# Kernel optimization log

Hardware: AMD Instinct MI355X
Metric: run time of the kernel (lower is better)

The kernel has to match this reference:

```python
import jax, jax.numpy as jnp
import numpy as np

N = 2048; E = 32768; E2 = 65536; B = 8; P = 20; M = B * P * P * P
NR = 16; SH = 9; FEAT = NR * SH; RE = 64; RH = 128; MC = 32; MH = 16; MODES = 10; CUT = 5.0


def _sh(u):
    # real spherical harmonics l=0,1,2, e3nn 'integral' normalization, on unit vectors u[...,3]
    x, y, z = u[..., 0], u[..., 1], u[..., 2]
    c0 = 0.28209479177387814  # 1/(2 sqrt(pi))
    c1 = 0.4886025119029199   # sqrt(3/(4 pi))
    l0 = jnp.full(x.shape, c0, dtype=u.dtype)
    return jnp.stack([
        l0,
        c1 * y, c1 * z, c1 * x,
        1.0925484305920792 * x * y,
        1.0925484305920792 * y * z,
        0.31539156525252005 * (3.0 * z * z - 1.0),
        1.0925484305920792 * x * z,
        0.5462742152960396 * (x * x - y * y),
    ], axis=-1)


def _gauss(r):
    # soft_one_hot_linspace(basis='gaussian', cutoff=False) * sqrt(RE)
    vals = jnp.linspace(0.0, CUT, RE)
    step = vals[1] - vals[0]
    d = (r[:, None] - vals) / step
    return jnp.exp(-d * d) / 1.12 * np.sqrt(RE)


def _norm_act(x):
    # NormActivation over irreps 16x0e + 16x1 + 16x2 (layout [16 | 16*3 | 16*5])
    s = x[:, :NR]
    v = x[:, NR:NR * 4].reshape(-1, NR, 3)
    t = x[:, NR * 4:].reshape(-1, NR, 5)
    s = s * jax.nn.sigmoid(jnp.abs(s))
    v = v * jax.nn.sigmoid(jnp.linalg.norm(v, axis=-1))[..., None]
    t = t * jax.nn.sigmoid(jnp.linalg.norm(t, axis=-1))[..., None]
    return jnp.concatenate([s, v.reshape(-1, NR * 3), t.reshape(-1, NR * 5)], axis=-1)


def _rmlp(e, m1, m2, m3):
    h = jax.nn.silu(e @ m1)
    h = jax.nn.silu(h @ m2)
    return h @ m3


def _gcn(src, dst, x, sh, emb_e, W, m1, m2, m3, n_dst, Wsc=None):
    # fully-connected tensor-product message passing: gather -> outer(feat, sh) -> GEMM
    # -> radial gate -> scatter-sum; optional self-connection
    xs = x[src]                                                    # [E, Cin]
    msg = (xs[:, :, None] * sh[:, None, :]).reshape(xs.shape[0], -1) @ W
    msg = msg * _rmlp(emb_e, m1, m2, m3)
    out = jax.ops.segment_sum(msg, dst, num_segments=n_dst)
    return out if Wsc is None else out + x @ Wsc


def _spec(x, wr, wi):
    # FNO-style 3D spectral conv on [B,P,P,P,C], low MODES kept in 4 corner blocks
    Px = x.shape[1]
    xf = jnp.fft.rfftn(x, axes=(1, 2, 3))
    w = wr + 1j * wi                                              # [4,C,C,m,m,m]
    m = MODES
    of = jnp.zeros(xf.shape, dtype=xf.dtype)
    corners = [(slice(0, m), slice(0, m)), (slice(-m, None), slice(0, m)),
               (slice(0, m), slice(-m, None)), (slice(-m, None), slice(-m, None))]
    for k, (s1, s2) in enumerate(corners):
        blk = jnp.einsum('bxyzi,ioxyz->bxyzo', xf[:, s1, s2, :m, :], w[k])
        of = of.at[:, s1, s2, :m, :].set(blk)
    return jnp.fft.irfftn(of, s=(Px, Px, Px), axes=(1, 2, 3))


def _forward(pos, cell, emb, g0_W, g0_Wsc, g0_m1, g0_m2, g0_m3,
             g12_W, g12_Wsc, g12_m1, g12_m2, g12_m3,
             a2m_W, a2m_m1, a2m_m2, a2m_m3,
             m2a_W, m2a_m1, m2a_m2, m2a_m3,
             fc0_W, fc0_b, sw_r, sw_i, pw, ff1, ff2, fc1, fc2,
             atomic_numbers, batch, edge_src, edge_dst, atom_src, mesh_dst):
    # atom-atom spherical GCN stack
    ev = pos[edge_src] - pos[edge_dst]
    el = jnp.linalg.norm(ev, axis=-1) + 1e-8
    sh_e = _sh(ev / el[:, None])
    emb_e = _gauss(el)
    x = emb[atomic_numbers]                                        # [N, NR]
    x = _gcn(edge_src, edge_dst, x, sh_e, emb_e, g0_W, g0_m1, g0_m2, g0_m3, N, g0_Wsc)
    for i in range(2):
        x = _norm_act(x)
        x = _gcn(edge_src, edge_dst, x, sh_e, emb_e, g12_W[i], g12_m1[i], g12_m2[i], g12_m3[i], N, g12_Wsc[i])
    # particle mesh positions per cell
    fr = jnp.arange(P) / P
    fg = jnp.stack(jnp.meshgrid(fr, fr, fr, indexing='ij'), axis=-1)   # [P,P,P,3]
    meshpos = jnp.einsum('xyzk,bkl->bxyzl', fg, cell).reshape(-1, 3)   # [M,3]
    # atom -> mesh conv
    ev2 = meshpos[mesh_dst] - pos[atom_src]
    el2 = jnp.linalg.norm(ev2, axis=-1) + 1e-8
    sh2 = _sh(ev2 / el2[:, None])
    emb2 = _gauss(el2)
    mf = _gcn(atom_src, mesh_dst, x, sh2, emb2, a2m_W, a2m_m1, a2m_m2, a2m_m3, M)   # [M, MC]
    mf = mf * jax.nn.sigmoid(jnp.abs(mf))                          # NormActivation on 0e
    mf = mf.reshape(B, P, P, P, MC)
    # PME / FNO mesh conv
    grid = jnp.broadcast_to(fg, (B, P, P, P, 3))
    h = jnp.concatenate([mf, grid], axis=-1) @ fc0_W + fc0_b       # lift to width MH
    for l in range(3):
        h = jax.nn.gelu(_spec(h, sw_r[l], sw_i[l]) + h @ pw[l])
        h = h + jax.nn.gelu(h @ ff1[l]) @ ff2[l]                   # using_ff branch
    h = jax.nn.gelu(h @ fc1) @ fc2                                 # [B,P,P,P,MH]
    mf2 = h.reshape(-1, MH)
    # mesh -> atom conv, per-atom energy, readout
    af = _gcn(mesh_dst, atom_src, mf2, sh2, emb2, m2a_W, m2a_m1, m2a_m2, m2a_m3, N)  # [N,1]
    return jax.ops.segment_sum(af, batch, num_segments=B)          # [B,1]


def setup_inputs():
    key = jax.random.key(0)
    ks = jax.random.split(key, 40)
    r = lambda i, shape, scale: jax.random.normal(ks[i], shape, dtype=jnp.float32) * scale
    inp = {}
    inp['pos'] = jax.random.uniform(ks[0], (N, 3), dtype=jnp.float32) * 10.0
    inp['cell'] = jnp.eye(3, dtype=jnp.float32)[None] * 10.0 + r(1, (B, 3, 3), 0.05)
    inp['atomic_numbers'] = jax.random.randint(ks[2], (N,), 1, 100)
    inp['batch'] = jnp.sort(jax.random.randint(ks[3], (N,), 0, B))
    inp['edge_src'] = jax.random.randint(ks[4], (E,), 0, N)
    inp['edge_dst'] = jax.random.randint(ks[5], (E,), 0, N)
    inp['atom_src'] = jax.random.randint(ks[6], (E2,), 0, N)
    inp['mesh_dst'] = jax.random.randint(ks[7], (E2,), 0, M)
    inp['emb'] = r(8, (100, NR), 1.0)
    inp['g0_W'] = r(9, (NR * SH, FEAT), (NR * SH) ** -0.5)
    inp['g0_Wsc'] = r(10, (NR, FEAT), NR ** -0.5)
    inp['g0_m1'] = r(11, (RE, RH), RE ** -0.5)
    inp['g0_m2'] = r(12, (RH, RH), RH ** -0.5)
    inp['g0_m3'] = r(13, (RH, FEAT), RH ** -0.5)
    inp['g12_W'] = r(14, (2, FEAT * SH, FEAT), (FEAT * SH) ** -0.5)
    inp['g12_Wsc'] = r(15, (2, FEAT, FEAT), FEAT ** -0.5)
    inp['g12_m1'] = r(16, (2, RE, RH), RE ** -0.5)
    inp['g12_m2'] = r(17, (2, RH, RH), RH ** -0.5)
    inp['g12_m3'] = r(18, (2, RH, FEAT), RH ** -0.5)
    inp['a2m_W'] = r(19, (FEAT * SH, MC), (FEAT * SH) ** -0.5)
    inp['a2m_m1'] = r(20, (RE, RH), RE ** -0.5)
    inp['a2m_m2'] = r(21, (RH, RH), RH ** -0.5)
    inp['a2m_m3'] = r(22, (RH, MC), RH ** -0.5)
    inp['m2a_W'] = r(23, (MH * SH, 1), (MH * SH) ** -0.5)
    inp['m2a_m1'] = r(24, (RE, RH), RE ** -0.5)
    inp['m2a_m2'] = r(25, (RH, RH), RH ** -0.5)
    inp['m2a_m3'] = r(26, (RH, 1), RH ** -0.5)
    inp['fc0_W'] = r(27, (MC + 3, MH), (MC + 3) ** -0.5)
    inp['fc0_b'] = jnp.zeros((MH,), dtype=jnp.float32)
    inp['sw_r'] = r(28, (3, 4, MH, MH, MODES, MODES, MODES), 1.0 / MH)
    inp['sw_i'] = r(29, (3, 4, MH, MH, MODES, MODES, MODES), 1.0 / MH)
    inp['pw'] = r(30, (3, MH, MH), MH ** -0.5)
    inp['ff1'] = r(31, (3, MH, 4 * MH), MH ** -0.5)
    inp['ff2'] = r(32, (3, 4 * MH, MH), (4 * MH) ** -0.5)
    inp['fc1'] = r(33, (MH, 128), MH ** -0.5)
    inp['fc2'] = r(34, (128, MH), 128 ** -0.5)
    return inp


def reference(pos, cell, emb, g0_W, g0_Wsc, g0_m1, g0_m2, g0_m3, g12_W, g12_Wsc, g12_m1, g12_m2, g12_m3, a2m_W, a2m_m1, a2m_m2, a2m_m3, m2a_W, m2a_m1, m2a_m2, m2a_m3, fc0_W, fc0_b, sw_r, sw_i, pw, ff1, ff2, fc1, fc2, atomic_numbers, batch, edge_src, edge_dst, atom_src, mesh_dst):
    return _forward(pos, cell, emb, g0_W, g0_Wsc, g0_m1, g0_m2, g0_m3, g12_W, g12_Wsc, g12_m1, g12_m2, g12_m3, a2m_W, a2m_m1, a2m_m2, a2m_m3, m2a_W, m2a_m1, m2a_m2, m2a_m3, fc0_W, fc0_b, sw_r, sw_i, pw, ff1, ff2, fc1, fc2, atomic_numbers, batch, edge_src, edge_dst, atom_src, mesh_dst)
```

## Files before the change

### kernel.cpp

```cpp
#include <hip/hip_runtime.h>
#include <math.h>

#define DEVI __device__ __forceinline__

namespace {

constexpr int N_  = 2048;
constexpr int E_  = 32768;
constexpr int E2_ = 65536;
constexpr int M_  = 64000;
constexpr int NT_ = 2048;
constexpr float TMAX_ = 5.5f;
constexpr float TH_ = TMAX_ / NT_;

DEVI float sigm(float x)  { return 1.0f/(1.0f+expf(-x)); }
DEVI float geluf(float x) {
  float t = tanhf(0.7978845608028654f*(x + 0.044715f*x*x*x));
  return 0.5f*x*(1.0f+t);
}

__global__ void zero_k(float* __restrict__ p, int n){
  int i = blockIdx.x*256 + threadIdx.x;
  if (i < n) p[i] = 0.0f;
}

__global__ void meshpos_k(const float* __restrict__ cell, float* __restrict__ mp){
  int m = blockIdx.x*256 + threadIdx.x;
  if (m >= M_) return;
  int b = m/8000, r = m%8000;
  float fx = (float)(r/400)    * 0.05f;
  float fy = (float)((r/20)%20)* 0.05f;
  float fz = (float)(r%20)     * 0.05f;
  const float* c = cell + b*9;
  mp[(size_t)m*3+0] = fx*c[0] + fy*c[3] + fz*c[6];
  mp[(size_t)m*3+1] = fx*c[1] + fy*c[4] + fz*c[7];
  mp[(size_t)m*3+2] = fx*c[2] + fy*c[5] + fz*c[8];
}

__global__ void edge_geom2_k(const float* __restrict__ Ppos, const int* __restrict__ pi,
                             const float* __restrict__ Qpos, const int* __restrict__ qi,
                             float* __restrict__ sh, float* __restrict__ el_out, int nE){
  int e = blockIdx.x*256 + threadIdx.x;
  if (e >= nE) return;
  int a = pi[e], b = qi[e];
  float ex = Ppos[(size_t)a*3+0] - Qpos[(size_t)b*3+0];
  float ey = Ppos[(size_t)a*3+1] - Qpos[(size_t)b*3+1];
  float ez = Ppos[(size_t)a*3+2] - Qpos[(size_t)b*3+2];
  float el = sqrtf(ex*ex+ey*ey+ez*ez) + 1e-8f;
  el_out[e] = el;
  float x = ex/el, y = ey/el, z = ez/el;
  float* s = sh + (size_t)e*9;
  s[0] = 0.28209479177387814f;
  s[1] = 0.4886025119029199f*y;
  s[2] = 0.4886025119029199f*z;
  s[3] = 0.4886025119029199f*x;
  s[4] = 1.0925484305920792f*x*y;
  s[5] = 1.0925484305920792f*y*z;
  s[6] = 0.31539156525252005f*(3.0f*z*z-1.0f);
  s[7] = 1.0925484305920792f*x*z;
  s[8] = 0.5462742152960396f*(x*x-y*y);
}

__global__ void gather_emb_k(const float* __restrict__ emb, const int* __restrict__ an,
                             float* __restrict__ x16){
  int idx = blockIdx.x*256 + threadIdx.x;
  if (idx >= N_*16) return;
  int n = idx >> 4, f = idx & 15;
  x16[idx] = emb[(size_t)an[n]*16 + f];
}

__global__ void es_k(float* __restrict__ Es){
  int idx = blockIdx.x*256 + threadIdx.x;
  if (idx >= NT_*64) return;
  int r = idx >> 6, k = idx & 63;
  const float step = 5.0f/63.0f;
  float d = (r*TH_ - k*step)/step;
  Es[idx] = expf(-d*d)*(8.0f/1.12f);
}

DEVI float lerp_tab(const float* __restrict__ T, float el, int O, int o){
  float u = el * (1.0f/TH_);
  u = fminf(u, (float)(NT_-1));
  int i = (int)u; if (i > NT_-2) i = NT_-2;
  float f = u - (float)i;
  float t0 = T[(size_t)i*O + o];
  float t1 = T[(size_t)(i+1)*O + o];
  return t0 + f*(t1 - t0);
}

struct BG {
  const float* A[5]; const float* B[5]; float* C[5];
  int K; int Nc[5];
};
template<int ACT>
__global__ __launch_bounds__(256) void bgemm_k(BG args){
  int chain = blockIdx.z;
  const float* A = args.A[chain];
  const float* Bm = args.B[chain];
  float* C = args.C[chain];
  int K = args.K, Nc = args.Nc[chain];
  int row0 = blockIdx.y*64, col0 = blockIdx.x*64;
  if (col0 >= Nc) return;
  __shared__ float As[16][72];
  __shared__ float Bs[16][72];
  int tid = threadIdx.x;
  int tx = tid & 15, ty = tid >> 4;
  float acc[4][4] = {};
  for (int k0 = 0; k0 < K; k0 += 16) {
    { int kk = tid & 15; int mloc = tid >> 4;
      int gk = k0 + kk;
      #pragma unroll
      for (int p = 0; p < 4; ++p) {
        int m = mloc + p*16; int gm = row0 + m;
        As[kk][m] = A[(size_t)gm*K + gk];
      } }
    { int nn = tid & 63; int kl = tid >> 6;
      #pragma unroll
      for (int p = 0; p < 4; ++p) {
        int kk = kl + p*4; int gk = k0 + kk; int gn = col0 + nn;
        Bs[kk][nn] = (gn < Nc) ? Bm[(size_t)gk*Nc + gn] : 0.0f;
      } }
    __syncthreads();
    #pragma unroll
    for (int kk = 0; kk < 16; ++kk) {
      float4 a4 = *(const float4*)&As[kk][ty*4];
      float4 b4 = *(const float4*)&Bs[kk][tx*4];
      float a[4] = {a4.x,a4.y,a4.z,a4.w};
      float b[4] = {b4.x,b4.y,b4.z,b4.w};
      #pragma unroll
      for (int i=0;i<4;++i)
        #pragma unroll
        for (int j=0;j<4;++j) acc[i][j] += a[i]*b[j];
    }
    __syncthreads();
  }
  for (int i=0;i<4;++i) {
    int gm = row0 + ty*4+i;
    for (int j=0;j<4;++j) {
      int gn = col0 + tx*4+j; if (gn >= Nc) continue;
      float v = acc[i][j];
      if (ACT==1) v = v*sigm(v);
      C[(size_t)gm*Nc + gn] = v;
    }
  }
}

__global__ __launch_bounds__(256) void gemm128_k(const float* __restrict__ A, const float* __restrict__ B,
                        float* __restrict__ C, int Mr, int K, int Nc){
  __shared__ float As[16][72];
  __shared__ float Bs[16][136];
  int tid = threadIdx.x;
  int row0 = blockIdx.y*64, col0 = blockIdx.x*128;
  int tx = tid & 15, ty = tid >> 4;
  float acc[4][8] = {};
  for (int k0 = 0; k0 < K; k0 += 16) {
    {
      int kk = tid & 15, mloc = tid >> 4;
      int gk = k0 + kk;
      #pragma unroll
      for (int p = 0; p < 4; ++p) {
        int m = mloc + p*16; int gm = row0 + m;
        As[kk][m] = (gm < Mr) ? A[(size_t)gm*K + gk] : 0.0f;
      }
    }
    {
      int nn4 = tid & 31, kk = tid >> 5;
      #pragma unroll
      for (int p = 0; p < 2; ++p) {
        int kkk = kk + p*8;
        int gk = k0 + kkk;
        int gn = col0 + nn4*4;
        float4 v = make_float4(0.f,0.f,0.f,0.f);
        if (gn + 3 < Nc) {
          v = *(const float4*)(B + (size_t)gk*Nc + gn);
        } else if (gn < Nc) {
          float t0 = B[(size_t)gk*Nc + gn];
          float t1 = (gn+1<Nc)? B[(size_t)gk*Nc + gn+1] : 0.f;
          float t2 = (gn+2<Nc)? B[(size_t)gk*Nc + gn+2] : 0.f;
          v = make_float4(t0,t1,t2,0.f);
        }
        *(float4*)&Bs[kkk][nn4*4] = v;
      }
    }
    __syncthreads();
    #pragma unroll
    for (int kk = 0; kk < 16; ++kk) {
      float4 a4 = *(const float4*)&As[kk][ty*4];
      float4 b0 = *(const float4*)&Bs[kk][tx*8];
      float4 b1 = *(const float4*)&Bs[kk][tx*8+4];
      float av[4] = {a4.x,a4.y,a4.z,a4.w};
      float bv[8] = {b0.x,b0.y,b0.z,b0.w,b1.x,b1.y,b1.z,b1.w};
      #pragma unroll
      for (int i=0;i<4;++i)
        #pragma unroll
        for (int j=0;j<8;++j) acc[i][j] += av[i]*bv[j];
    }
    __syncthreads();
  }
  for (int i=0;i<4;++i){
    int gm = row0 + ty*4 + i; if (gm >= Mr) continue;
    for (int j=0;j<8;++j){
      int gn = col0 + tx*8 + j; if (gn >= Nc) continue;
      C[(size_t)gm*Nc + gn] = acc[i][j];
    }
  }
}

template<int O>
__global__ void wreshape_k(const float* __restrict__ W, float* __restrict__ Wt, int F){
  int idx = blockIdx.x*256 + threadIdx.x;
  int total = F*9*O;
  if (idx >= total) return;
  int o = idx % O; int s = (idx / O) % 9; int f = idx / (9*O);
  Wt[idx] = W[(size_t)(f*9+s)*O + o];
}

template<int O>
__global__ void econtract_k(const float* __restrict__ Y, const int* __restrict__ src,
                            const int* __restrict__ dst, const float* __restrict__ SH,
                            const float* __restrict__ EL, const float* __restrict__ T,
                            float* __restrict__ out, int nE){
  int idx = blockIdx.x*256 + threadIdx.x;
  if (idx >= nE*O) return;
  int e = idx / O, o = idx - e*O;
  const float* sr = SH + (size_t)e*9;
  const float* yr = Y + (size_t)src[e]*(9*O) + o;
  float acc = 0.0f;
  #pragma unroll
  for (int s = 0; s < 9; ++s) acc += sr[s] * yr[s*O];
  float rv = lerp_tab(T, EL[e], O, o);
  atomicAdd(&out[(size_t)dst[e]*O + o], acc * rv);
}

__global__ void normact_k(const float* __restrict__ x, float* __restrict__ y){
  int idx = blockIdx.x*256 + threadIdx.x;
  if (idx >= N_*16) return;
  int n = idx >> 4, r = idx & 15;
  const float* xr = x + (size_t)n*144;
  float* yr = y + (size_t)n*144;
  float s = xr[r];
  yr[r] = s * sigm(fabsf(s));
  float v0 = xr[16+r*3], v1 = xr[16+r*3+1], v2 = xr[16+r*3+2];
  float gv = sigm(sqrtf(v0*v0+v1*v1+v2*v2));
  yr[16+r*3]=v0*gv; yr[16+r*3+1]=v1*gv; yr[16+r*3+2]=v2*gv;
  float t0=xr[64+r*5],t1=xr[64+r*5+1],t2=xr[64+r*5+2],t3=xr[64+r*5+3],t4=xr[64+r*5+4];
  float gt = sigm(sqrtf(t0*t0+t1*t1+t2*t2+t3*t3+t4*t4));
  yr[64+r*5]=t0*gt; yr[64+r*5+1]=t1*gt; yr[64+r*5+2]=t2*gt; yr[64+r*5+3]=t3*gt; yr[64+r*5+4]=t4*gt;
}

__global__ void fc0_k(const float* __restrict__ mf, const float* __restrict__ Wt,
                      const float* __restrict__ bb, float* __restrict__ h){
  int idx = blockIdx.x*256 + threadIdx.x;
  if (idx >= M_*16) return;
  int m = idx >> 4, o = idx & 15;
  int r = m % 8000;
  float fx = (float)(r/400)*0.05f, fy = (float)((r/20)%20)*0.05f, fz = (float)(r%20)*0.05f;
  const float* mfr = mf + (size_t)m*32;
  float acc = bb[o];
  #pragma unroll
  for (int j=0;j<32;++j){
    float v = mfr[j];
    v = v * sigm(fabsf(v));
    acc += v*Wt[j*16+o];
  }
  acc += fx*Wt[32*16+o] + fy*Wt[33*16+o] + fz*Wt[34*16+o];
  h[idx] = acc;
}

__global__ __launch_bounds__(256) void wreorder2_k(const float* __restrict__ wr, const float* __restrict__ wi,
                          float2* __restrict__ W2){
  __shared__ float2 tile[2560];
  int l = blockIdx.y;
  const float* wrl = wr + (size_t)l*1024000;
  const float* wil = wi + (size_t)l*1024000;
  int p = blockIdx.x;
  int ky = p/20, kx = p%20;
  int corner = ((kx>=10)?1:0) + ((ky>=10)?2:0);
  int base2 = corner*256;
  int soff = (kx%10)*100 + (ky%10)*10;
  for (int t = threadIdx.x; t < 2560; t += 256){
    int chunk = t/10, kz = t - chunk*10;
    size_t src = (size_t)(base2 + chunk)*1000 + soff + kz;
    tile[kz*256 + chunk] = make_float2(wrl[src], wil[src]);
  }
  __syncthreads();
  float2* dst = W2 + (size_t)l*1024000 + (size_t)p*2560;
  for (int t = threadIdx.x; t < 2560; t += 256) dst[t] = tile[t];
}

__global__ __launch_bounds__(256) void zyfwd_k(const float* __restrict__ h, float2* __restrict__ cA){
  __shared__ float  pl[20][20][4];
  __shared__ float2 tz[20][10][4];
  __shared__ float2 tw[20];
  int tid = threadIdx.x;
  if (tid < 20){ float a = -6.283185307179586f*tid/20.0f; tw[tid] = make_float2(cosf(a), sinf(a)); }
  int bid = blockIdx.x;
  int b = bid / 80, rem = bid % 80;
  int X = rem >> 2, cg = rem & 3;
  const float* hp = h + (size_t)(b*20+X)*400*16 + cg*4;
  for (int t = tid; t < 400; t += 256) {
    int y = t/20, z = t%20;
    const float4 v = *(const float4*)(hp + (size_t)t*16);
    pl[y][z][0]=v.x; pl[y][z][1]=v.y; pl[y][z][2]=v.z; pl[y][z][3]=v.w;
  }
  __syncthreads();
  for (int t = tid; t < 800; t += 256) {
    int c = t & 3, kz = (t>>2)%10, y = t/40;
    float sr=0.0f, si=0.0f; int j=0;
    for (int z=0; z<20; ++z){
      float v = pl[y][z][c];
      float2 w = tw[j];
      sr += v*w.x; si += v*w.y;
      j += kz; if (j>=20) j-=20;
    }
    tz[y][kz][c] = make_float2(sr,si);
  }
  __syncthreads();
  for (int t = tid; t < 800; t += 256) {
    int c = t & 3, kz = (t>>2)%10, ky = t/40;
    float sr=0.0f, si=0.0f; int j=0;
    for (int y=0; y<20; ++y){
      float2 v = tz[y][kz][c];
      float2 w = tw[j];
      sr += v.x*w.x - v.y*w.y;
      si += v.x*w.y + v.y*w.x;
      j += ky; if (j>=20) j-=20;
    }
    cA[((size_t)((b*20+ky)*10+kz)*20 + X)*16 + cg*4+c] = make_float2(sr,si);
  }
}

__global__ __launch_bounds__(256) void xmix_k(const float2* __restrict__ cA, float2* __restrict__ cB,
                    const float2* __restrict__ W2){
  __shared__ float2 xin[16][20];
  __shared__ float2 Xf[20][16];
  __shared__ float2 Mx[20][16];
  __shared__ float2 twf[20], twi[20];
  int tid = threadIdx.x;
  if (tid < 20){
    float a = -6.283185307179586f*tid/20.0f;
    twf[tid] = make_float2(cosf(a), sinf(a));
    twi[tid] = make_float2(cosf(a), -sinf(a));
  }
  int bid = blockIdx.x;
  int b = bid/200, rem = bid%200;
  int ky = rem/10, kz = rem%10;
  const float2* src = cA + (size_t)((b*20+ky)*10+kz)*320;
  for (int t = tid; t < 320; t += 256){
    int x = t/16, i = t%16;
    xin[i][x] = src[t];
  }
  __syncthreads();
  for (int t = tid; t < 320; t += 256){
    int kx = t/16, i = t%16;
    float sr=0.0f, si=0.0f; int j=0;
    for (int x=0;x<20;++x){
      float2 v = xin[i][x]; float2 w = twf[j];
      sr += v.x*w.x - v.y*w.y; si += v.x*w.y + v.y*w.x;
      j += kx; if (j>=20) j-=20;
    }
    Xf[kx][i] = make_float2(sr,si);
  }
  __syncthreads();
  for (int t = tid; t < 320; t += 256){
    int kx = t/16, o = t%16;
    const float2* wp = W2 + ((size_t)(ky*20+kx)*10 + kz)*256 + o;
    float sr=0.0f, si=0.0f;
    #pragma unroll
    for (int i=0;i<16;++i){
      float2 a = Xf[kx][i];
      float2 w = wp[i*16];
      sr += a.x*w.x - a.y*w.y;
      si += a.x*w.y + a.y*w.x;
    }
    Mx[kx][o] = make_float2(sr,si);
  }
  __syncthreads();
  for (int t = tid; t < 320; t += 256){
    int x = t/16, o = t%16;
    float sr=0.0f, si=0.0f; int j=0;
    for (int kx=0;kx<20;++kx){
      float2 v = Mx[kx][o]; float2 w = twi[j];
      sr += v.x*w.x - v.y*w.y; si += v.x*w.y + v.y*w.x;
      j += x; if (j>=20) j-=20;
    }
    cB[((size_t)((b*20+x)*20+ky)*10+kz)*16 + o] = make_float2(sr,si);
  }
}

__global__ __launch_bounds__(256) void yzinv_k(const float2* __restrict__ cB, float* __restrict__ spec){
  __shared__ float2 ci[20][10][4];
  __shared__ float2 ty[20][10][4];
  __shared__ float2 twi[20];
  int tid = threadIdx.x;
  if (tid < 20){ float a = 6.283185307179586f*tid/20.0f; twi[tid] = make_float2(cosf(a), sinf(a)); }
  int bid = blockIdx.x;
  int b = bid/80, rem = bid%80;
  int X = rem>>2, cg = rem&3;
  const float2* src = cB + (size_t)(b*20+X)*200*16;
  for (int t = tid; t < 800; t += 256){
    int c = t&3, kz = (t>>2)%10, ky = t/40;
    ci[ky][kz][c] = src[(size_t)(ky*10+kz)*16 + cg*4+c];
  }
  __syncthreads();
  for (int t = tid; t < 800; t += 256){
    int c = t&3, kz = (t>>2)%10, y = t/40;
    float sr=0.0f, si=0.0f; int j=0;
    for (int ky=0;ky<20;++ky){
      float2 v = ci[ky][kz][c]; float2 w = twi[j];
      sr += v.x*w.x - v.y*w.y; si += v.x*w.y + v.y*w.x;
      j += y; if (j>=20) j-=20;
    }
    ty[y][kz][c] = make_float2(sr,si);
  }
  __syncthreads();
  float* dst = spec + (size_t)(b*20+X)*400*16 + cg*4;
  for (int t = tid; t < 1600; t += 256){
    int c = t&3, z = (t>>2)%20, y = t/80;
    float acc = ty[y][0][c].x;
    float a2 = 0.0f; int jj = 0;
    for (int kz=1; kz<10; ++kz){
      jj += z; if (jj>=20) jj-=20;
      float2 v = ty[y][kz][c]; float2 w = twi[jj];
      a2 += v.x*w.x - v.y*w.y;
    }
    acc += 2.0f*a2;
    dst[(size_t)(y*20+z)*16 + c] = acc * (1.0f/8000.0f);
  }
}

__global__ __launch_bounds__(256) void ffn3_k(const float* __restrict__ spec, const float* __restrict__ h,
                     const float* __restrict__ pw, const float* __restrict__ ff1,
                     const float* __restrict__ ff2, float* __restrict__ hout){
  __shared__ float spw[256];
  __shared__ float sf1[1024];
  __shared__ float sf2[1024];
  __shared__ float h2s[128][17];
  __shared__ float red[2][128][17];
  int tid = threadIdx.x;
  spw[tid] = pw[tid];
  for (int t = tid; t < 1024; t += 256){ sf1[t]=ff1[t]; sf2[t]=ff2[t]; }
  int rl = tid >> 1, q = tid & 1;
  int m = blockIdx.x*128 + rl;
  const float* hr = h + (size_t)m*16;
  float hl[16];
  #pragma unroll
  for (int i=0;i<16;++i) hl[i] = hr[i];
  __syncthreads();
  const float* sp = spec + (size_t)m*16;
  #pragma unroll
  for (int c=0;c<8;++c){
    int o = q*8+c;
    float acc = sp[o];
    #pragma unroll
    for (int i=0;i<16;++i) acc += hl[i]*spw[i*16+o];
    h2s[rl][o] = geluf(acc);
  }
  __syncthreads();
  float h2l[16];
  #pragma unroll
  for (int i=0;i<16;++i) h2l[i] = h2s[rl][i];
  float part[16] = {};
  for (int kk=0;kk<32;++kk){
    int k = q*32+kk;
    float a0=0.0f, a1=0.0f;
    #pragma unroll
    for (int i=0;i<8;++i){ a0 += h2l[i]*sf1[i*64+k]; a1 += h2l[8+i]*sf1[(8+i)*64+k]; }
    float tk = geluf(a0+a1);
    #pragma unroll
    for (int o=0;o<16;++o) part[o] += tk*sf2[k*16+o];
  }
  #pragma unroll
  for (int o=0;o<16;++o) red[q][rl][o] = part[o];
  __syncthreads();
  #pragma unroll
  for (int c=0;c<8;++c){
    int o = q*8+c;
    hout[(size_t)m*16+o] = h2s[rl][o] + red[0][rl][o] + red[1][rl][o];
  }
}

__global__ __launch_bounds__(256) void fctail3_k(const float* __restrict__ h, const float* __restrict__ fc1,
                        const float* __restrict__ fc2, float* __restrict__ outm){
  __shared__ float s1[2048];
  __shared__ float s2[2048];
  __shared__ float red[2][128][17];
  int tid = threadIdx.x;
  for (int t = tid; t < 2048; t += 256){ s1[t]=fc1[t]; s2[t]=fc2[t]; }
  int rl = tid >> 1, q = tid & 1;
  int m = blockIdx.x*128 + rl;
  const float* hr = h + (size_t)m*16;
  float hl[16];
  #pragma unroll
  for (int i=0;i<16;++i) hl[i] = hr[i];
  __syncthreads();
  float part[16] = {};
  for (int kk=0;kk<64;++kk){
    int k = q*64+kk;
    float a0=0.0f, a1=0.0f;
    #pragma unroll
    for (int i=0;i<8;++i){ a0 += hl[i]*s1[i*128+k]; a1 += hl[8+i]*s1[(8+i)*128+k]; }
    float tk = geluf(a0+a1);
    #pragma unroll
    for (int o=0;o<16;++o) part[o] += tk*s2[k*16+o];
  }
  #pragma unroll
  for (int o=0;o<16;++o) red[q][rl][o] = part[o];
  __syncthreads();
  #pragma unroll
  for (int c=0;c<8;++c){
    int o = q*8+c;
    outm[(size_t)m*16+o] = red[0][rl][o] + red[1][rl][o];
  }
}

__global__ void m2a_k(const float* __restrict__ mf2, const int* __restrict__ mdst,
                      const int* __restrict__ asrc, const float* __restrict__ sh2,
                      const float* __restrict__ Wt, const float* __restrict__ EL,
                      const float* __restrict__ T, float* __restrict__ af){
  int e = blockIdx.x*256 + threadIdx.x;
  if (e >= E2_) return;
  const float* xr = mf2 + (size_t)mdst[e]*16;
  const float* sr = sh2 + (size_t)e*9;
  float sh[9];
  #pragma unroll
  for (int s=0;s<9;++s) sh[s] = sr[s];
  float acc = 0.0f;
  #pragma unroll
  for (int f=0;f<16;++f) {
    float xv = xr[f];
    float dot = 0.0f;
    #pragma unroll
    for (int s=0;s<9;++s) dot += sh[s]*Wt[f*9+s];
    acc += xv*dot;
  }
  float rv = lerp_tab(T, EL[e], 1, 0);
  atomicAdd(&af[asrc[e]], acc*rv);
}

__global__ void bsum_k(const float* __restrict__ af, const int* __restrict__ batch,
                       float* __restrict__ out){
  int n = blockIdx.x*256 + threadIdx.x;
  if (n >= N_) return;
  atomicAdd(&out[batch[n]], af[n]);
}

}

extern "C" void kernel_launch(void* const* d_in, const int* in_sizes, int n_in,
                              void* d_out, int out_size, void* d_ws, size_t ws_size,
                              hipStream_t stream) {
  (void)in_sizes; (void)n_in; (void)out_size; (void)ws_size;
  const float* pos   = (const float*)d_in[0];
  const float* cell  = (const float*)d_in[1];
  const int*   an    = (const int*)d_in[2];
  const int*   batch = (const int*)d_in[3];
  const int*   esrc  = (const int*)d_in[4];
  const int*   edst  = (const int*)d_in[5];
  const int*   asrc  = (const int*)d_in[6];
  const int*   mdst  = (const int*)d_in[7];
  const float* emb   = (const float*)d_in[8];
  const float* g0_W  = (const float*)d_in[9];
  const float* g0_Wsc= (const float*)d_in[10];
  const float* g0_m1 = (const float*)d_in[11];
  const float* g0_m2 = (const float*)d_in[12];
  const float* g0_m3 = (const float*)d_in[13];
  const float* g12_W = (const float*)d_in[14];
  const float* g12_Wsc=(const float*)d_in[15];
  const float* g12_m1= (const float*)d_in[16];
  const float* g12_m2= (const float*)d_in[17];
  const float* g12_m3= (const float*)d_in[18];
  const float* a2m_W = (const float*)d_in[19];
  const float* a2m_m1= (const float*)d_in[20];
  const float* a2m_m2= (const float*)d_in[21];
  const float* a2m_m3= (const float*)d_in[22];
  const float* m2a_W = (const float*)d_in[23];
  const float* m2a_m1= (const float*)d_in[24];
  const float* m2a_m2= (const float*)d_in[25];
  const float* m2a_m3= (const float*)d_in[26];
  const float* fc0_W = (const float*)d_in[27];
  const float* fc0_b = (const float*)d_in[28];
  const float* sw_r  = (const float*)d_in[29];
  const float* sw_i  = (const float*)d_in[30];
  const float* pw    = (const float*)d_in[31];
  const float* ff1   = (const float*)d_in[32];
  const float* ff2   = (const float*)d_in[33];
  const float* fc1   = (const float*)d_in[34];
  const float* fc2   = (const float*)d_in[35];
  float* out = (float*)d_out;

  float* Wp = (float*)d_ws;
  size_t off = 0;
  auto alloc = [&](size_t n){ float* p = Wp + off; off += n; return p; };
  float* meshpos = alloc((size_t)M_*3);
  float* she   = alloc((size_t)E_*9);
  float* ELe   = alloc((size_t)E_);
  float* sh2   = alloc((size_t)E2_*9);
  float* EL2   = alloc((size_t)E2_);
  float* x16   = alloc((size_t)N_*16);
  float* xatom = alloc((size_t)N_*144);
  float* xact  = alloc((size_t)N_*144);
  float* Wt    = alloc((size_t)144*1296);
  float* Yg    = alloc((size_t)N_*1296);
  float* mf    = alloc((size_t)M_*32);
  float* hbuf  = alloc((size_t)M_*16);
  float* htmp  = alloc((size_t)M_*16);
  float2* cA   = (float2*)alloc(1024000);
  float2* cB   = (float2*)alloc(1024000);
  float2* W2   = (float2*)alloc((size_t)3*2048000);
  float* af    = alloc((size_t)N_);
  float* Es    = alloc((size_t)NT_*64);
  float* H1g   = alloc((size_t)5*NT_*128);
  float* H2g   = alloc((size_t)5*NT_*128);
  float* T0    = alloc((size_t)NT_*144);
  float* T1    = alloc((size_t)NT_*144);
  float* T2    = alloc((size_t)NT_*144);
  float* T3    = alloc((size_t)NT_*32);
  float* T4    = alloc((size_t)NT_*1);

  auto g1 = [](int n){ return dim3((unsigned)((n+255)/256)); };
  auto gg2 = [](int Mr, int Nc){ return dim3((unsigned)((Nc+127)/128), (unsigned)((Mr+63)/64)); };

  zero_k<<<g1(8), 256, 0, stream>>>(out, 8);
  zero_k<<<g1(N_), 256, 0, stream>>>(af, N_);
  zero_k<<<g1(M_*32), 256, 0, stream>>>(mf, M_*32);

  meshpos_k<<<g1(M_), 256, 0, stream>>>(cell, meshpos);
  edge_geom2_k<<<g1(E_), 256, 0, stream>>>(pos, esrc, pos, edst, she, ELe, E_);
  edge_geom2_k<<<g1(E2_), 256, 0, stream>>>(meshpos, mdst, pos, asrc, sh2, EL2, E2_);
  gather_emb_k<<<g1(N_*16), 256, 0, stream>>>(emb, an, x16);

  wreorder2_k<<<dim3(400,3), 256, 0, stream>>>(sw_r, sw_i, W2);

  {
    es_k<<<g1(NT_*64), 256, 0, stream>>>(Es);
    BG l1, l2, l3;
    const float* m1s[5] = {g0_m1, g12_m1, g12_m1+(size_t)64*128, a2m_m1, m2a_m1};
    const float* m2s[5] = {g0_m2, g12_m2, g12_m2+(size_t)128*128, a2m_m2, m2a_m2};
    const float* m3s[5] = {g0_m3, g12_m3, g12_m3+(size_t)128*144, a2m_m3, m2a_m3};
    float* Ts[5] = {T0, T1, T2, T3, T4};
    int NOs[5] = {144, 144, 144, 32, 1};
    for (int c = 0; c < 5; ++c) {
      l1.A[c] = Es;                      l1.B[c] = m1s[c]; l1.C[c] = H1g + (size_t)c*NT_*128; l1.Nc[c] = 128;
      l2.A[c] = H1g + (size_t)c*NT_*128; l2.B[c] = m2s[c]; l2.C[c] = H2g + (size_t)c*NT_*128; l2.Nc[c] = 128;
      l3.A[c] = H2g + (size_t)c*NT_*128; l3.B[c] = m3s[c]; l3.C[c] = Ts[c];                   l3.Nc[c] = NOs[c];
    }
    l1.K = 64; l2.K = 128; l3.K = 128;
    bgemm_k<1><<<dim3(2, NT_/64, 5), 256, 0, stream>>>(l1);
    bgemm_k<1><<<dim3(2, NT_/64, 5), 256, 0, stream>>>(l2);
    bgemm_k<0><<<dim3(3, NT_/64, 5), 256, 0, stream>>>(l3);
  }

  wreshape_k<144><<<g1(16*9*144), 256, 0, stream>>>(g0_W, Wt, 16);
  gemm128_k<<<gg2(N_,1296), 256, 0, stream>>>(x16, Wt, Yg, N_, 16, 1296);
  gemm128_k<<<gg2(N_,144), 256, 0, stream>>>(x16, g0_Wsc, xatom, N_, 16, 144);
  econtract_k<144><<<g1(E_*144), 256, 0, stream>>>(Yg, esrc, edst, she, ELe, T0, xatom, E_);

  for (int i = 0; i < 2; ++i) {
    normact_k<<<g1(N_*16), 256, 0, stream>>>(xatom, xact);
    wreshape_k<144><<<g1(144*9*144), 256, 0, stream>>>(g12_W + (size_t)i*1296*144, Wt, 144);
    gemm128_k<<<gg2(N_,1296), 256, 0, stream>>>(xact, Wt, Yg, N_, 144, 1296);
    gemm128_k<<<gg2(N_,144), 256, 0, stream>>>(xact, g12_Wsc + (size_t)i*144*144, xatom, N_, 144, 144);
    econtract_k<144><<<g1(E_*144), 256, 0, stream>>>(Yg, esrc, edst, she, ELe, (i==0)?T1:T2, xatom, E_);
  }

  wreshape_k<32><<<g1(144*9*32), 256, 0, stream>>>(a2m_W, Wt, 144);
  gemm128_k<<<gg2(N_,288), 256, 0, stream>>>(xatom, Wt, Yg, N_, 144, 288);
  econtract_k<32><<<g1(E2_*32), 256, 0, stream>>>(Yg, asrc, mdst, sh2, EL2, T3, mf, E2_);

  fc0_k<<<g1(M_*16), 256, 0, stream>>>(mf, fc0_W, fc0_b, hbuf);
  for (int l = 0; l < 3; ++l) {
    zyfwd_k<<<dim3(640), 256, 0, stream>>>(hbuf, cA);
    xmix_k<<<dim3(1600), 256, 0, stream>>>(cA, cB, W2 + (size_t)l*1024000);
    yzinv_k<<<dim3(640), 256, 0, stream>>>(cB, htmp);
    ffn3_k<<<dim3(500), 256, 0, stream>>>(htmp, hbuf, pw + (size_t)l*256,
                                          ff1 + (size_t)l*1024, ff2 + (size_t)l*1024, hbuf);
  }
  fctail3_k<<<dim3(500), 256, 0, stream>>>(hbuf, fc1, fc2, htmp);

  m2a_k<<<g1(E2_), 256, 0, stream>>>(htmp, mdst, asrc, sh2, m2a_W, EL2, T4, af);
  bsum_k<<<g1(N_), 256, 0, stream>>>(af, batch, out);
}
```

Before: 610.4 us.

## Replace FP32 atom GEMMs with split-bf16 MFMA GEMMs and fused normact conversion

The shared-memory FP32 tiled GEMM for the atom-side tensor-product layers is replaced by a one-wave-per-16x16-tile MFMA kernel. It emulates FP32 precision with a three-product hi/lo bf16 split. Inputs are converted into padded K-major bf16 hi/lo buffers by new conversion kernels, and the normact kernel now writes the split bf16 form directly. This moves the GEMM work onto matrix cores at the cost of extra conversion passes, reduced precision versus true FP32, and a simple kernel with no shared-memory reuse.

```diff
diff --git a/kernel.cpp b/kernel.cpp
--- a/kernel.cpp
+++ b/kernel.cpp
@@ -13,10 +13,24 @@
 constexpr float TMAX_ = 5.5f;
 constexpr float TH_ = TMAX_ / NT_;
 
+using bf16x8 = __attribute__((ext_vector_type(8))) short;
+using f32x4  = __attribute__((ext_vector_type(4))) float;
+
 DEVI float sigm(float x)  { return 1.0f/(1.0f+expf(-x)); }
 DEVI float geluf(float x) {
   float t = tanhf(0.7978845608028654f*(x + 0.044715f*x*x*x));
   return 0.5f*x*(1.0f+t);
+}
+
+DEVI unsigned short bf16rn(float x){
+  unsigned u = __float_as_uint(x);
+  unsigned r = u + 0x7FFFu + ((u>>16)&1u);
+  return (unsigned short)(r>>16);
+}
+DEVI void bf16split(float x, unsigned short& h, unsigned short& l){
+  h = bf16rn(x);
+  float hf = __uint_as_float(((unsigned)h)<<16);
+  l = bf16rn(x - hf);
 }
 
 __global__ void zero_k(float* __restrict__ p, int n){
@@ -145,74 +159,99 @@
   }
 }
 
-__global__ __launch_bounds__(256) void gemm128_k(const float* __restrict__ A, const float* __restrict__ B,
-                        float* __restrict__ C, int Mr, int K, int Nc){
-  __shared__ float As[16][72];
-  __shared__ float Bs[16][136];
-  int tid = threadIdx.x;
-  int row0 = blockIdx.y*64, col0 = blockIdx.x*128;
-  int tx = tid & 15, ty = tid >> 4;
-  float acc[4][8] = {};
-  for (int k0 = 0; k0 < K; k0 += 16) {
-    {
-      int kk = tid & 15, mloc = tid >> 4;
-      int gk = k0 + kk;
-      #pragma unroll
-      for (int p = 0; p < 4; ++p) {
-        int m = mloc + p*16; int gm = row0 + m;
-        As[kk][m] = (gm < Mr) ? A[(size_t)gm*K + gk] : 0.0f;
-      }
-    }
-    {
-      int nn4 = tid & 31, kk = tid >> 5;
-      #pragma unroll
-      for (int p = 0; p < 2; ++p) {
-        int kkk = kk + p*8;
-        int gk = k0 + kkk;
-        int gn = col0 + nn4*4;
-        float4 v = make_float4(0.f,0.f,0.f,0.f);
-        if (gn + 3 < Nc) {
-          v = *(const float4*)(B + (size_t)gk*Nc + gn);
-        } else if (gn < Nc) {
-          float t0 = B[(size_t)gk*Nc + gn];
-          float t1 = (gn+1<Nc)? B[(size_t)gk*Nc + gn+1] : 0.f;
-          float t2 = (gn+2<Nc)? B[(size_t)gk*Nc + gn+2] : 0.f;
-          v = make_float4(t0,t1,t2,0.f);
-        }
-        *(float4*)&Bs[kkk][nn4*4] = v;
-      }
-    }
-    __syncthreads();
-    #pragma unroll
-    for (int kk = 0; kk < 16; ++kk) {
-      float4 a4 = *(const float4*)&As[kk][ty*4];
-      float4 b0 = *(const float4*)&Bs[kk][tx*8];
-      float4 b1 = *(const float4*)&Bs[kk][tx*8+4];
-      float av[4] = {a4.x,a4.y,a4.z,a4.w};
-      float bv[8] = {b0.x,b0.y,b0.z,b0.w,b1.x,b1.y,b1.z,b1.w};
-      #pragma unroll
-      for (int i=0;i<4;++i)
-        #pragma unroll
-        for (int j=0;j<8;++j) acc[i][j] += av[i]*bv[j];
-    }
-    __syncthreads();
-  }
-  for (int i=0;i<4;++i){
-    int gm = row0 + ty*4 + i; if (gm >= Mr) continue;
-    for (int j=0;j<8;++j){
-      int gn = col0 + tx*8 + j; if (gn >= Nc) continue;
-      C[(size_t)gm*Nc + gn] = acc[i][j];
-    }
-  }
+__global__ void convA_k(const float* __restrict__ x, unsigned short* __restrict__ hi,
+                        unsigned short* __restrict__ lo, int Mr, int K, int KP){
+  int idx = blockIdx.x*256 + threadIdx.x;
+  if (idx >= Mr*KP) return;
+  int n = idx / KP, k = idx - n*KP;
+  unsigned short h = 0, l = 0;
+  if (k < K) bf16split(x[(size_t)n*K + k], h, l);
+  hi[idx] = h; lo[idx] = l;
+}
+
+__global__ void convT_k(const float* __restrict__ B, unsigned short* __restrict__ hi,
+                        unsigned short* __restrict__ lo, int K, int Nc, int KP){
+  int idx = blockIdx.x*256 + threadIdx.x;
+  if (idx >= Nc*KP) return;
+  int n = idx / KP, k = idx - n*KP;
+  unsigned short h = 0, l = 0;
+  if (k < K) bf16split(B[(size_t)k*Nc + n], h, l);
+  hi[idx] = h; lo[idx] = l;
 }
 
 template<int O>
-__global__ void wreshape_k(const float* __restrict__ W, float* __restrict__ Wt, int F){
+__global__ void wreshapeT_k(const float* __restrict__ W, unsigned short* __restrict__ hi,
+                            unsigned short* __restrict__ lo, int F, int KP){
   int idx = blockIdx.x*256 + threadIdx.x;
-  int total = F*9*O;
+  int total = 9*O*KP;
   if (idx >= total) return;
-  int o = idx % O; int s = (idx / O) % 9; int f = idx / (9*O);
-  Wt[idx] = W[(size_t)(f*9+s)*O + o];
+  int n = idx / KP, f = idx - n*KP;
+  unsigned short h = 0, l = 0;
+  if (f < F){
+    int s = n / O, o = n - s*O;
+    bf16split(W[(size_t)(f*9+s)*O + o], h, l);
+  }
+  hi[idx] = h; lo[idx] = l;
+}
+
+__global__ void normact_bf_k(const float* __restrict__ x, unsigned short* __restrict__ hi,
+                             unsigned short* __restrict__ lo){
+  int idx = blockIdx.x*256 + threadIdx.x;
+  if (idx >= N_*16) return;
+  int n = idx >> 4, r = idx & 15;
+  const float* xr = x + (size_t)n*144;
+  unsigned short* hr = hi + (size_t)n*160;
+  unsigned short* lr = lo + (size_t)n*160;
+  unsigned short h, l;
+  float s = xr[r];
+  bf16split(s * sigm(fabsf(s)), h, l); hr[r]=h; lr[r]=l;
+  float v0 = xr[16+r*3], v1 = xr[16+r*3+1], v2 = xr[16+r*3+2];
+  float gv = sigm(sqrtf(v0*v0+v1*v1+v2*v2));
+  bf16split(v0*gv,h,l); hr[16+r*3]=h;   lr[16+r*3]=l;
+  bf16split(v1*gv,h,l); hr[16+r*3+1]=h; lr[16+r*3+1]=l;
+  bf16split(v2*gv,h,l); hr[16+r*3+2]=h; lr[16+r*3+2]=l;
+  float t0=xr[64+r*5],t1=xr[64+r*5+1],t2=xr[64+r*5+2],t3=xr[64+r*5+3],t4=xr[64+r*5+4];
+  float gt = sigm(sqrtf(t0*t0+t1*t1+t2*t2+t3*t3+t4*t4));
+  bf16split(t0*gt,h,l); hr[64+r*5]=h;   lr[64+r*5]=l;
+  bf16split(t1*gt,h,l); hr[64+r*5+1]=h; lr[64+r*5+1]=l;
+  bf16split(t2*gt,h,l); hr[64+r*5+2]=h; lr[64+r*5+2]=l;
+  bf16split(t3*gt,h,l); hr[64+r*5+3]=h; lr[64+r*5+3]=l;
+  bf16split(t4*gt,h,l); hr[64+r*5+4]=h; lr[64+r*5+4]=l;
+  hr[144+r] = 0; lr[144+r] = 0;
+}
+
+__global__ __launch_bounds__(256) void mgemm_k(const unsigned short* __restrict__ Ah,
+                     const unsigned short* __restrict__ Al,
+                     const unsigned short* __restrict__ BTh,
+                     const unsigned short* __restrict__ Bl,
+                     float* __restrict__ C, int Mr, int KP, int Nc){
+  int tilesN = Nc >> 4;
+  int wid = ((blockIdx.x*256 + threadIdx.x) >> 6);
+  int tm = wid / tilesN, tn = wid - tm*tilesN;
+  if (tm*16 >= Mr) return;
+  int lane = threadIdx.x & 63;
+  int l15 = lane & 15;
+  int kb  = (lane >> 4) * 8;
+  const unsigned short* ah = Ah + (size_t)(tm*16 + l15)*KP + kb;
+  const unsigned short* al = Al + (size_t)(tm*16 + l15)*KP + kb;
+  const unsigned short* bh = BTh + (size_t)(tn*16 + l15)*KP + kb;
+  const unsigned short* bl = Bl  + (size_t)(tn*16 + l15)*KP + kb;
+  f32x4 acc = {0.f,0.f,0.f,0.f};
+  for (int k0 = 0; k0 < KP; k0 += 32) {
+    bf16x8 a_h = *(const bf16x8*)(ah + k0);
+    bf16x8 a_l = *(const bf16x8*)(al + k0);
+    bf16x8 b_h = *(const bf16x8*)(bh + k0);
+    bf16x8 b_l = *(const bf16x8*)(bl + k0);
+    acc = __builtin_amdgcn_mfma_f32_16x16x32_bf16(a_h, b_h, acc, 0, 0, 0);
+    acc = __builtin_amdgcn_mfma_f32_16x16x32_bf16(a_h, b_l, acc, 0, 0, 0);
+    acc = __builtin_amdgcn_mfma_f32_16x16x32_bf16(a_l, b_h, acc, 0, 0, 0);
+  }
+  int r0 = tm*16 + (lane>>4)*4;
+  int co = tn*16 + l15;
+  #pragma unroll
+  for (int r = 0; r < 4; ++r){
+    C[(size_t)(r0+r)*Nc + co] = acc[r];
+  }
 }
 
 template<int O>
@@ -230,22 +269,6 @@
   for (int s = 0; s < 9; ++s) acc += sr[s] * yr[s*O];
   float rv = lerp_tab(T, EL[e], O, o);
   atomicAdd(&out[(size_t)dst[e]*O + o], acc * rv);
-}
-
-__global__ void normact_k(const float* __restrict__ x, float* __restrict__ y){
-  int idx = blockIdx.x*256 + threadIdx.x;
-  if (idx >= N_*16) return;
-  int n = idx >> 4, r = idx & 15;
-  const float* xr = x + (size_t)n*144;
-  float* yr = y + (size_t)n*144;
-  float s = xr[r];
-  yr[r] = s * sigm(fabsf(s));
-  float v0 = xr[16+r*3], v1 = xr[16+r*3+1], v2 = xr[16+r*3+2];
-  float gv = sigm(sqrtf(v0*v0+v1*v1+v2*v2));
-  yr[16+r*3]=v0*gv; yr[16+r*3+1]=v1*gv; yr[16+r*3+2]=v2*gv;
-  float t0=xr[64+r*5],t1=xr[64+r*5+1],t2=xr[64+r*5+2],t3=xr[64+r*5+3],t4=xr[64+r*5+4];
-  float gt = sigm(sqrtf(t0*t0+t1*t1+t2*t2+t3*t3+t4*t4));
-  yr[64+r*5]=t0*gt; yr[64+r*5+1]=t1*gt; yr[64+r*5+2]=t2*gt; yr[64+r*5+3]=t3*gt; yr[64+r*5+4]=t4*gt;
 }
 
 __global__ void fc0_k(const float* __restrict__ mf, const float* __restrict__ Wt,
@@ -591,7 +614,7 @@
 
   float* Wp = (float*)d_ws;
   size_t off = 0;
-  auto alloc = [&](size_t n){ float* p = Wp + off; off += n; return p; };
+  auto alloc = [&](size_t n){ off = (off+3)&~(size_t)3; float* p = Wp + off; off += n; return p; };
   float* meshpos = alloc((size_t)M_*3);
   float* she   = alloc((size_t)E_*9);
   float* ELe   = alloc((size_t)E_);
@@ -599,8 +622,6 @@
   float* EL2   = alloc((size_t)E2_);
   float* x16   = alloc((size_t)N_*16);
   float* xatom = alloc((size_t)N_*144);
-  float* xact  = alloc((size_t)N_*144);
-  float* Wt    = alloc((size_t)144*1296);
   float* Yg    = alloc((size_t)N_*1296);
   float* mf    = alloc((size_t)M_*32);
   float* hbuf  = alloc((size_t)M_*16);
@@ -617,9 +638,16 @@
   float* T2    = alloc((size_t)NT_*144);
   float* T3    = alloc((size_t)NT_*32);
   float* T4    = alloc((size_t)NT_*1);
+  unsigned short* Ah  = (unsigned short*)alloc((size_t)N_*160/2);
+  unsigned short* Al  = (unsigned short*)alloc((size_t)N_*160/2);
+  unsigned short* BTh = (unsigned short*)alloc((size_t)1296*160/2);
+  unsigned short* BTl = (unsigned short*)alloc((size_t)1296*160/2);
+  unsigned short* BWh = (unsigned short*)alloc((size_t)144*160/2);
+  unsigned short* BWl = (unsigned short*)alloc((size_t)144*160/2);
 
   auto g1 = [](int n){ return dim3((unsigned)((n+255)/256)); };
-  auto gg2 = [](int Mr, int Nc){ return dim3((unsigned)((Nc+127)/128), (unsigned)((Mr+63)/64)); };
+  auto mg = [](int tiles){ return dim3((unsigned)((tiles+3)/4)); };
+  const int TM = N_/16;
 
   zero_k<<<g1(8), 256, 0, stream>>>(out, 8);
   zero_k<<<g1(N_), 256, 0, stream>>>(af, N_);
@@ -651,21 +679,25 @@
     bgemm_k<0><<<dim3(3, NT_/64, 5), 256, 0, stream>>>(l3);
   }
 
-  wreshape_k<144><<<g1(16*9*144), 256, 0, stream>>>(g0_W, Wt, 16);
-  gemm128_k<<<gg2(N_,1296), 256, 0, stream>>>(x16, Wt, Yg, N_, 16, 1296);
-  gemm128_k<<<gg2(N_,144), 256, 0, stream>>>(x16, g0_Wsc, xatom, N_, 16, 144);
+  convA_k<<<g1(N_*32), 256, 0, stream>>>(x16, Ah, Al, N_, 16, 32);
+  wreshapeT_k<144><<<g1(9*144*32), 256, 0, stream>>>(g0_W, BTh, BTl, 16, 32);
+  convT_k<<<g1(144*32), 256, 0, stream>>>(g0_Wsc, BWh, BWl, 16, 144, 32);
+  mgemm_k<<<mg(TM*81), 256, 0, stream>>>(Ah, Al, BTh, BTl, Yg, N_, 32, 1296);
+  mgemm_k<<<mg(TM*9),  256, 0, stream>>>(Ah, Al, BWh, BWl, xatom, N_, 32, 144);
   econtract_k<144><<<g1(E_*144), 256, 0, stream>>>(Yg, esrc, edst, she, ELe, T0, xatom, E_);
 
   for (int i = 0; i < 2; ++i) {
-    normact_k<<<g1(N_*16), 256, 0, stream>>>(xatom, xact);
-    wreshape_k<144><<<g1(144*9*144), 256, 0, stream>>>(g12_W + (size_t)i*1296*144, Wt, 144);
-    gemm128_k<<<gg2(N_,1296), 256, 0, stream>>>(xact, Wt, Yg, N_, 144, 1296);
-    gemm128_k<<<gg2(N_,144), 256, 0, stream>>>(xact, g12_Wsc + (size_t)i*144*144, xatom, N_, 144, 144);
+    normact_bf_k<<<g1(N_*16), 256, 0, stream>>>(xatom, Ah, Al);
+    wreshapeT_k<144><<<g1(9*144*160), 256, 0, stream>>>(g12_W + (size_t)i*1296*144, BTh, BTl, 144, 160);
+    convT_k<<<g1(144*160), 256, 0, stream>>>(g12_Wsc + (size_t)i*144*144, BWh, BWl, 144, 144, 160);
+    mgemm_k<<<mg(TM*81), 256, 0, stream>>>(Ah, Al, BTh, BTl, Yg, N_, 160, 1296);
+    mgemm_k<<<mg(TM*9),  256, 0, stream>>>(Ah, Al, BWh, BWl, xatom, N_, 160, 144);
     econtract_k<144><<<g1(E_*144), 256, 0, stream>>>(Yg, esrc, edst, she, ELe, (i==0)?T1:T2, xatom, E_);
   }
 
-  wreshape_k<32><<<g1(144*9*32), 256, 0, stream>>>(a2m_W, Wt, 144);
-  gemm128_k<<<gg2(N_,288), 256, 0, stream>>>(xatom, Wt, Yg, N_, 144, 288);
+  convA_k<<<g1(N_*160), 256, 0, stream>>>(xatom, Ah, Al, N_, 144, 160);
+  wreshapeT_k<32><<<g1(9*32*160), 256, 0, stream>>>(a2m_W, BTh, BTl, 144, 160);
+  mgemm_k<<<mg(TM*18), 256, 0, stream>>>(Ah, Al, BTh, BTl, Yg, N_, 160, 288);
   econtract_k<32><<<g1(E2_*32), 256, 0, stream>>>(Yg, asrc, mdst, sh2, EL2, T3, mf, E2_);
 
   fc0_k<<<g1(M_*16), 256, 0, stream>>>(mf, fc0_W, fc0_b, hbuf);
```

Result: faster. 509.3 us (-16.6%).
